# Performance work log

Measured on AMD Instinct MI355X. Metric: run time of the kernel, lower is better.

The kernel has to match this reference:

```python
import jax, jax.numpy as jnp
import numpy as np

N_NODES = 100000


def setup_inputs() -> dict:
    key = jax.random.key(0)
    k1, k2, k3 = jax.random.split(key, 3)
    embedding = jax.random.normal(k1, (N_NODES, 128), dtype=jnp.float32)
    # xavier-ish scale for 128-dim fan-in
    weights = jax.random.normal(k2, (2, 4, 128, 128), dtype=jnp.float32) * 0.088
    biases = jnp.zeros((2, 4, 128), dtype=jnp.float32)
    edges = jax.random.randint(k3, (4, 2, 150000), 0, N_NODES, dtype=jnp.int32)
    return {"embedding": embedding, "weights": weights, "biases": biases, "edges": edges}


def _hetero_conv(h, W, b, edges, n_nodes):
    """HeteroGraphConv(mean) over R relations; each GraphConv uses norm='both'.
    h: [N, d_in], W: [R, d_in, d_h], b: [R, d_h], edges: [R, 2, E]."""

    def per_rel(e, Wr, br):
        src, dst = e[0], e[1]
        ones = jnp.ones(src.shape, dtype=h.dtype)
        deg_out = jnp.maximum(jax.ops.segment_sum(ones, src, num_segments=n_nodes), 1.0)
        deg_in = jnp.maximum(jax.ops.segment_sum(ones, dst, num_segments=n_nodes), 1.0)
        # D_src^{-1/2} X W
        x = h * jax.lax.rsqrt(deg_out)[:, None]
        m = x @ Wr  # [N, d_h]
        # gather along edges, scatter-add to dst (A @ m)
        agg = jax.ops.segment_sum(m[src], dst, num_segments=n_nodes)
        return agg * jax.lax.rsqrt(deg_in)[:, None] + br

    outs = jax.vmap(per_rel)(edges, W, b)  # [R, N, d_h]
    return outs.mean(axis=0)


def reference(embedding, weights, biases, edges):
    n_nodes = embedding.shape[0]
    num_layers = weights.shape[0]
    h = embedding
    for i in range(num_layers):
        out = _hetero_conv(h, weights[i], biases[i], edges, n_nodes)
        out = jax.nn.leaky_relu(out, negative_slope=0.2)
        if i > 0:
            out = out + h  # residual (hidden == in, slice [:, :hidden] is identity)
        h = out
    return h
```

## Files before the change

### kernel.cpp

```cpp
#include <hip/hip_runtime.h>
#include <cstdint>
#include <cstddef>

#define N_NODES 100000
#define D 128
#define R 4
#define NE 150000
#define LAYERS 2
#define NROWS (R * N_NODES)
#define CAP 16
#define OVFS 12
#define TILES (N_NODES / 16)
#define GRID 256
#define TPB 512

typedef __attribute__((ext_vector_type(8))) short bf16x8;
typedef __attribute__((ext_vector_type(4))) float f32x4;
typedef __attribute__((ext_vector_type(4))) int i32x4;
typedef __attribute__((ext_vector_type(4))) unsigned short u16x4;

__device__ __forceinline__ unsigned short f2bf(float x) {
  union { float f; unsigned int u; } v; v.f = x;
  unsigned int u = v.u;
  return (unsigned short)((u + 0x7fffu + ((u >> 16) & 1u)) >> 16);
}
__device__ __forceinline__ float bf2f(unsigned short u) {
  union { unsigned int i; float f; } v; v.i = ((unsigned int)u) << 16;
  return v.f;
}

__global__ void prep1_kernel(const float* __restrict__ emb, const float* __restrict__ W,
                             const float* __restrict__ biases, const int* __restrict__ edges,
                             int* __restrict__ deg_i, unsigned short* __restrict__ hb,
                             unsigned short* __restrict__ Wt, float* __restrict__ bmean) {
  int t = blockIdx.x * blockDim.x + threadIdx.x;
  if (t < N_NODES * D / 4) {
    f32x4 v = *(const f32x4*)(emb + (size_t)t * 4);
    u16x4 o;
#pragma unroll
    for (int j = 0; j < 4; ++j) o[j] = f2bf(v[j]);
    *(u16x4*)(hb + (size_t)t * 4) = o;
  }
  if (t < NE * R) {
    int r = t / NE;
    int e = t - r * NE;
    int src = edges[(size_t)(r * 2) * NE + e];
    atomicAdd(&deg_i[r * N_NODES + src], 1);
  }
  if (t < LAYERS * R * D * D) {
    int k = t & 127;
    int c = (t >> 7) & 127;
    int lr = t >> 14;
    Wt[((size_t)lr << 14) | (c << 7) | k] = f2bf(W[((size_t)lr << 14) | (k << 7) | c]);
  }
  if (t < LAYERS * D) {
    int l = t >> 7, cc = t & 127;
    float s = 0.f;
    for (int r = 0; r < R; ++r) s += biases[((size_t)l * R + r) * D + cc];
    bmean[t] = s * 0.25f;
  }
}

__global__ void fill_kernel(const int* __restrict__ edges, const int* __restrict__ deg_i,
                            int* __restrict__ cursor, int2* __restrict__ rec2,
                            int2* __restrict__ ovf) {
  int e = blockIdx.x * blockDim.x + threadIdx.x;
  int r = blockIdx.y;
  if (e >= NE) return;
  int src = edges[(size_t)(r * 2) * NE + e];
  int dst = edges[(size_t)(r * 2 + 1) * NE + e];
  float sc = rsqrtf(fmaxf((float)deg_i[r * N_NODES + src], 1.0f));
  int rowg = r * N_NODES + dst;
  int slot = atomicAdd(&cursor[rowg], 1);
  if (slot < 4) {
    rec2[(((size_t)(r * TILES + (dst >> 4)) * 16 + (dst & 15)) << 2) + slot] =
        make_int2(src, __float_as_int(sc));
  } else if (slot < CAP) {
    ovf[(size_t)rowg * OVFS + (slot - 4)] = make_int2(src, __float_as_int(sc));
  }
}

__global__ __launch_bounds__(TPB, 2) void fused_kernel(
    const unsigned short* __restrict__ hb,
    const int2* __restrict__ rec2,
    const int2* __restrict__ ovf,
    const int* __restrict__ cnt,
    const unsigned short* __restrict__ Wt,
    const float* __restrict__ bmean,
    const unsigned short* __restrict__ resid_bf,
    float* __restrict__ out_f,
    unsigned short* __restrict__ out_bf) {
  __shared__ unsigned short t_lds[2][R * 4 * 64 * 8];
  const int w = threadIdx.x >> 6;
  const int lane = threadIdx.x & 63;
  const int m = lane & 15;
  const int q = lane >> 4;
  const int bid = blockIdx.x;
  const int nt = (TILES - bid + GRID - 1) / GRID;

  if (w < 4) {
    const int r = w;
    for (int it = 0; it < nt + 1; ++it) {
      if (it < nt) {
        const int tile = bid + it * GRID;
        const int rowg = r * N_NODES + tile * 16 + m;
        const int2* rp = rec2 + (((size_t)(r * TILES + tile) * 16 + m) << 2);
        int n = cnt[rowg];
        n = (n > CAP) ? CAP : n;
        i32x4 r01 = *(const i32x4*)(rp);
        i32x4 r23 = *(const i32x4*)(rp + 2);
        int   srcs[4] = { r01.x, r01.z, r23.x, r23.z };
        float scs[4]  = { __int_as_float(r01.y), __int_as_float(r01.w),
                          __int_as_float(r23.y), __int_as_float(r23.w) };
#pragma unroll
        for (int e = 0; e < 4; ++e) {
          if (e >= n) { srcs[e] = 0; scs[e] = 0.f; }
        }
        float accf[4][8];
#pragma unroll
        for (int ks = 0; ks < 4; ++ks)
#pragma unroll
          for (int j = 0; j < 8; ++j) accf[ks][j] = 0.f;
#pragma unroll
        for (int e = 0; e < 4; ++e) {
          const unsigned short* hp = hb + (size_t)srcs[e] * D + q * 8;
#pragma unroll
          for (int ks = 0; ks < 4; ++ks) {
            bf16x8 a = *(const bf16x8*)(hp + ks * 32);
#pragma unroll
            for (int j = 0; j < 8; ++j)
              accf[ks][j] += scs[e] * bf2f((unsigned short)a[j]);
          }
        }
        if (__builtin_expect(n > 4, 0)) {
          const int2* op = ovf + (size_t)rowg * OVFS;
          for (int i = 4; i < n; i += 2) {
            i32x4 rr = *(const i32x4*)(op + (i - 4));
            bool pairOk = (i + 1) < n;
            int  sA = rr.x;
            int  sB = pairOk ? rr.z : 0;
            float c0 = __int_as_float(rr.y);
            float c1 = pairOk ? __int_as_float(rr.w) : 0.f;
            const unsigned short* h0 = hb + (size_t)sA * D + q * 8;
            const unsigned short* h1 = hb + (size_t)sB * D + q * 8;
#pragma unroll
            for (int ks = 0; ks < 4; ++ks) {
              bf16x8 a0 = *(const bf16x8*)(h0 + ks * 32);
              bf16x8 a1 = *(const bf16x8*)(h1 + ks * 32);
#pragma unroll
              for (int j = 0; j < 8; ++j)
                accf[ks][j] += c0 * bf2f((unsigned short)a0[j]) + c1 * bf2f((unsigned short)a1[j]);
            }
          }
        }
        unsigned short* dstp = &t_lds[it & 1][(((r * 4) << 6) + lane) * 8];
#pragma unroll
        for (int ks = 0; ks < 4; ++ks) {
          union { bf16x8 v; unsigned short s[8]; } u;
#pragma unroll
          for (int j = 0; j < 8; ++j) u.s[j] = f2bf(accf[ks][j]);
          *(bf16x8*)(dstp + (ks << 6) * 8) = u.v;
        }
      }
      __syncthreads();
    }
  } else {
    const int cw = w - 4;
    bf16x8 breg[R][4][2];
#pragma unroll
    for (int r = 0; r < R; ++r) {
      const unsigned short* wr = Wt + ((size_t)r << 14);
#pragma unroll
      for (int ks = 0; ks < 4; ++ks)
#pragma unroll
        for (int c = 0; c < 2; ++c) {
          int ct = cw * 2 + c;
          breg[r][ks][c] = *(const bf16x8*)(wr + ((ct * 16 + m) << 7) + ks * 32 + q * 8);
        }
    }
    for (int it = 0; it < nt + 1; ++it) {
      if (it > 0) {
        const int tile = bid + (it - 1) * GRID;
        const int pb = (it - 1) & 1;
        float oacc[2][4];
#pragma unroll
        for (int c = 0; c < 2; ++c)
#pragma unroll
          for (int i = 0; i < 4; ++i) oacc[c][i] = 0.f;
#pragma unroll
        for (int r = 0; r < R; ++r) {
          f32x4 acc2[2];
#pragma unroll
          for (int c = 0; c < 2; ++c) acc2[c] = (f32x4){0.f, 0.f, 0.f, 0.f};
#pragma unroll
          for (int ks = 0; ks < 4; ++ks) {
            bf16x8 a = *(const bf16x8*)&t_lds[pb][(((r * 4 + ks) << 6) + lane) * 8];
#pragma unroll
            for (int c = 0; c < 2; ++c)
              acc2[c] = __builtin_amdgcn_mfma_f32_16x16x32_bf16(a, breg[r][ks][c], acc2[c], 0, 0, 0);
          }
          i32x4 ci = *(const i32x4*)(cnt + (size_t)r * N_NODES + tile * 16 + q * 4);
#pragma unroll
          for (int c = 0; c < 2; ++c)
#pragma unroll
            for (int i = 0; i < 4; ++i)
              oacc[c][i] += rsqrtf(fmaxf((float)ci[i], 1.0f)) * acc2[c][i];
        }
#pragma unroll
        for (int c = 0; c < 2; ++c) {
          int colx = (cw * 2 + c) * 16 + m;
          float bm = bmean[colx];
#pragma unroll
          for (int i = 0; i < 4; ++i) {
            int row = tile * 16 + q * 4 + i;
            float v = oacc[c][i] * 0.25f + bm;
            v = (v >= 0.f) ? v : 0.2f * v;
            if (resid_bf) v += bf2f(resid_bf[(size_t)row * D + colx]);
            if (out_f) out_f[(size_t)row * D + colx] = v;
            else       out_bf[(size_t)row * D + colx] = f2bf(v);
          }
        }
      }
      __syncthreads();
    }
  }
}

extern "C" void kernel_launch(void* const* d_in, const int* in_sizes, int n_in,
                              void* d_out, int out_size, void* d_ws, size_t ws_size,
                              hipStream_t stream) {
  const float* emb    = (const float*)d_in[0];
  const float* W      = (const float*)d_in[1];
  const float* biases = (const float*)d_in[2];
  const int*   edges  = (const int*)d_in[3];
  float* out = (float*)d_out;
  char* ws = (char*)d_ws;

  size_t off = 0;
  auto alloc = [&](size_t bytes) { size_t o = off; off += (bytes + 255) & ~255ull; return o; };
  int* ints      = (int*)(ws + alloc((size_t)2 * NROWS * 4));
  int* deg_i     = ints;
  int* cursor    = ints + NROWS;
  size_t zero_bytes = off;
  int2* rec2     = (int2*)(ws + alloc((size_t)R * TILES * 16 * 4 * 8));
  int2* ovf      = (int2*)(ws + alloc((size_t)NROWS * OVFS * 8));
  unsigned short* hb  = (unsigned short*)(ws + alloc((size_t)N_NODES * D * 2));
  unsigned short* hb2 = (unsigned short*)(ws + alloc((size_t)N_NODES * D * 2));
  unsigned short* Wt  = (unsigned short*)(ws + alloc((size_t)LAYERS * R * D * D * 2));
  float* bmean   = (float*)(ws + alloc((size_t)LAYERS * D * 4));
  (void)ws_size;

  hipMemsetAsync(ws, 0, zero_bytes, stream);
  prep1_kernel<<<(N_NODES * D / 4 + 255) / 256, 256, 0, stream>>>(
      emb, W, biases, edges, deg_i, hb, Wt, bmean);
  fill_kernel<<<dim3((NE + 255) / 256, R), 256, 0, stream>>>(edges, deg_i, cursor, rec2, ovf);

  fused_kernel<<<GRID, TPB, 0, stream>>>(
      hb, rec2, ovf, cursor, Wt, bmean, nullptr, nullptr, hb2);
  fused_kernel<<<GRID, TPB, 0, stream>>>(
      hb2, rec2, ovf, cursor, Wt + (size_t)R * D * D, bmean + D, hb2, out, nullptr);
}
```

Baseline: 340.1 us.

## Split fused warp-specialized kernel into separate aggregation and GEMM kernels

Replaces the warp-specialized fused kernel, where four gather waves fed four MFMA waves through double-buffered LDS, with two kernels. A fully parallel aggregation kernel writes bf16 aggregates for every relation to a global buffer, and a GEMM kernel then reads them back. The in-degree scaling moves into the aggregation step so the GEMM can accumulate across relations directly. This removes per-tile __syncthreads coupling and raises occupancy for the gather, at the cost of about 100MB of extra global traffic per layer plus two more launches.

```diff
diff --git a/kernel.cpp b/kernel.cpp
--- a/kernel.cpp
+++ b/kernel.cpp
@@ -11,8 +11,8 @@
 #define CAP 16
 #define OVFS 12
 #define TILES (N_NODES / 16)
-#define GRID 256
-#define TPB 512
+#define AGG_BLOCKS ((R * TILES) / 8)
+#define GEMM_BLOCKS 1024
 
 typedef __attribute__((ext_vector_type(8))) short bf16x8;
 typedef __attribute__((ext_vector_type(4))) float f32x4;
@@ -80,148 +80,138 @@
   }
 }
 
-__global__ __launch_bounds__(TPB, 2) void fused_kernel(
-    const unsigned short* __restrict__ hb,
+__global__ __launch_bounds__(512, 4) void agg_kernel(
+    const unsigned short* __restrict__ hin,
     const int2* __restrict__ rec2,
     const int2* __restrict__ ovf,
     const int* __restrict__ cnt,
+    unsigned short* __restrict__ agg) {
+  const int gw = (blockIdx.x * blockDim.x + threadIdx.x) >> 6;
+  const int lane = threadIdx.x & 63;
+  const int m = lane & 15;
+  const int q = lane >> 4;
+  const int rel = gw / TILES;
+  const int tile = gw - rel * TILES;
+
+  const int rowg = rel * N_NODES + tile * 16 + m;
+  const int2* rp = rec2 + (((size_t)gw * 16 + m) << 2);
+  int cn = cnt[rowg];
+  int n = cn > CAP ? CAP : cn;
+  float sin_ = rsqrtf(fmaxf((float)cn, 1.0f));
+  i32x4 r01 = *(const i32x4*)(rp);
+  i32x4 r23 = *(const i32x4*)(rp + 2);
+  int   srcs[4] = { r01.x, r01.z, r23.x, r23.z };
+  float scs[4]  = { __int_as_float(r01.y), __int_as_float(r01.w),
+                    __int_as_float(r23.y), __int_as_float(r23.w) };
+#pragma unroll
+  for (int e = 0; e < 4; ++e) {
+    if (e >= n) { srcs[e] = 0; scs[e] = 0.f; }
+  }
+  float accf[4][8];
+#pragma unroll
+  for (int ks = 0; ks < 4; ++ks)
+#pragma unroll
+    for (int j = 0; j < 8; ++j) accf[ks][j] = 0.f;
+#pragma unroll
+  for (int e = 0; e < 4; ++e) {
+    const unsigned short* hp = hin + (size_t)srcs[e] * D + q * 8;
+#pragma unroll
+    for (int ks = 0; ks < 4; ++ks) {
+      bf16x8 a = *(const bf16x8*)(hp + ks * 32);
+#pragma unroll
+      for (int j = 0; j < 8; ++j)
+        accf[ks][j] += scs[e] * bf2f((unsigned short)a[j]);
+    }
+  }
+  if (__builtin_expect(n > 4, 0)) {
+    const int2* op = ovf + (size_t)rowg * OVFS;
+    for (int i = 4; i < n; i += 2) {
+      i32x4 rr = *(const i32x4*)(op + (i - 4));
+      bool pairOk = (i + 1) < n;
+      int  sA = rr.x;
+      int  sB = pairOk ? rr.z : 0;
+      float c0 = __int_as_float(rr.y);
+      float c1 = pairOk ? __int_as_float(rr.w) : 0.f;
+      const unsigned short* h0 = hin + (size_t)sA * D + q * 8;
+      const unsigned short* h1 = hin + (size_t)sB * D + q * 8;
+#pragma unroll
+      for (int ks = 0; ks < 4; ++ks) {
+        bf16x8 a0 = *(const bf16x8*)(h0 + ks * 32);
+        bf16x8 a1 = *(const bf16x8*)(h1 + ks * 32);
+#pragma unroll
+        for (int j = 0; j < 8; ++j)
+          accf[ks][j] += c0 * bf2f((unsigned short)a0[j]) + c1 * bf2f((unsigned short)a1[j]);
+      }
+    }
+  }
+  unsigned short* dstp = agg + (((size_t)gw * 4) * 64 + lane) * 8;
+#pragma unroll
+  for (int ks = 0; ks < 4; ++ks) {
+    union { bf16x8 v; unsigned short s[8]; } u;
+#pragma unroll
+    for (int j = 0; j < 8; ++j) u.s[j] = f2bf(accf[ks][j] * sin_);
+    *(bf16x8*)(dstp + (size_t)ks * 64 * 8) = u.v;
+  }
+}
+
+__global__ __launch_bounds__(256, 2) void gemm_kernel(
+    const unsigned short* __restrict__ agg,
     const unsigned short* __restrict__ Wt,
     const float* __restrict__ bmean,
     const unsigned short* __restrict__ resid_bf,
     float* __restrict__ out_f,
     unsigned short* __restrict__ out_bf) {
-  __shared__ unsigned short t_lds[2][R * 4 * 64 * 8];
   const int w = threadIdx.x >> 6;
   const int lane = threadIdx.x & 63;
   const int m = lane & 15;
   const int q = lane >> 4;
-  const int bid = blockIdx.x;
-  const int nt = (TILES - bid + GRID - 1) / GRID;
-
-  if (w < 4) {
-    const int r = w;
-    for (int it = 0; it < nt + 1; ++it) {
-      if (it < nt) {
-        const int tile = bid + it * GRID;
-        const int rowg = r * N_NODES + tile * 16 + m;
-        const int2* rp = rec2 + (((size_t)(r * TILES + tile) * 16 + m) << 2);
-        int n = cnt[rowg];
-        n = (n > CAP) ? CAP : n;
-        i32x4 r01 = *(const i32x4*)(rp);
-        i32x4 r23 = *(const i32x4*)(rp + 2);
-        int   srcs[4] = { r01.x, r01.z, r23.x, r23.z };
-        float scs[4]  = { __int_as_float(r01.y), __int_as_float(r01.w),
-                          __int_as_float(r23.y), __int_as_float(r23.w) };
-#pragma unroll
-        for (int e = 0; e < 4; ++e) {
-          if (e >= n) { srcs[e] = 0; scs[e] = 0.f; }
-        }
-        float accf[4][8];
-#pragma unroll
-        for (int ks = 0; ks < 4; ++ks)
-#pragma unroll
-          for (int j = 0; j < 8; ++j) accf[ks][j] = 0.f;
-#pragma unroll
-        for (int e = 0; e < 4; ++e) {
-          const unsigned short* hp = hb + (size_t)srcs[e] * D + q * 8;
-#pragma unroll
-          for (int ks = 0; ks < 4; ++ks) {
-            bf16x8 a = *(const bf16x8*)(hp + ks * 32);
-#pragma unroll
-            for (int j = 0; j < 8; ++j)
-              accf[ks][j] += scs[e] * bf2f((unsigned short)a[j]);
-          }
-        }
-        if (__builtin_expect(n > 4, 0)) {
-          const int2* op = ovf + (size_t)rowg * OVFS;
-          for (int i = 4; i < n; i += 2) {
-            i32x4 rr = *(const i32x4*)(op + (i - 4));
-            bool pairOk = (i + 1) < n;
-            int  sA = rr.x;
-            int  sB = pairOk ? rr.z : 0;
-            float c0 = __int_as_float(rr.y);
-            float c1 = pairOk ? __int_as_float(rr.w) : 0.f;
-            const unsigned short* h0 = hb + (size_t)sA * D + q * 8;
-            const unsigned short* h1 = hb + (size_t)sB * D + q * 8;
-#pragma unroll
-            for (int ks = 0; ks < 4; ++ks) {
-              bf16x8 a0 = *(const bf16x8*)(h0 + ks * 32);
-              bf16x8 a1 = *(const bf16x8*)(h1 + ks * 32);
-#pragma unroll
-              for (int j = 0; j < 8; ++j)
-                accf[ks][j] += c0 * bf2f((unsigned short)a0[j]) + c1 * bf2f((unsigned short)a1[j]);
-            }
-          }
-        }
-        unsigned short* dstp = &t_lds[it & 1][(((r * 4) << 6) + lane) * 8];
-#pragma unroll
-        for (int ks = 0; ks < 4; ++ks) {
-          union { bf16x8 v; unsigned short s[8]; } u;
-#pragma unroll
-          for (int j = 0; j < 8; ++j) u.s[j] = f2bf(accf[ks][j]);
-          *(bf16x8*)(dstp + (ks << 6) * 8) = u.v;
-        }
-      }
-      __syncthreads();
-    }
-  } else {
-    const int cw = w - 4;
-    bf16x8 breg[R][4][2];
+
+  bf16x8 breg[R][4][2];
+#pragma unroll
+  for (int r = 0; r < R; ++r) {
+    const unsigned short* wr = Wt + ((size_t)r << 14);
+#pragma unroll
+    for (int ks = 0; ks < 4; ++ks)
+#pragma unroll
+      for (int c = 0; c < 2; ++c) {
+        int ct = w * 2 + c;
+        breg[r][ks][c] = *(const bf16x8*)(wr + ((ct * 16 + m) << 7) + ks * 32 + q * 8);
+      }
+  }
+
+  for (int tile = blockIdx.x; tile < TILES; tile += GEMM_BLOCKS) {
+    f32x4 acc[2];
+#pragma unroll
+    for (int c = 0; c < 2; ++c) acc[c] = (f32x4){0.f, 0.f, 0.f, 0.f};
 #pragma unroll
     for (int r = 0; r < R; ++r) {
-      const unsigned short* wr = Wt + ((size_t)r << 14);
-#pragma unroll
-      for (int ks = 0; ks < 4; ++ks)
-#pragma unroll
-        for (int c = 0; c < 2; ++c) {
-          int ct = cw * 2 + c;
-          breg[r][ks][c] = *(const bf16x8*)(wr + ((ct * 16 + m) << 7) + ks * 32 + q * 8);
-        }
-    }
-    for (int it = 0; it < nt + 1; ++it) {
-      if (it > 0) {
-        const int tile = bid + (it - 1) * GRID;
-        const int pb = (it - 1) & 1;
-        float oacc[2][4];
-#pragma unroll
-        for (int c = 0; c < 2; ++c)
-#pragma unroll
-          for (int i = 0; i < 4; ++i) oacc[c][i] = 0.f;
-#pragma unroll
-        for (int r = 0; r < R; ++r) {
-          f32x4 acc2[2];
-#pragma unroll
-          for (int c = 0; c < 2; ++c) acc2[c] = (f32x4){0.f, 0.f, 0.f, 0.f};
-#pragma unroll
-          for (int ks = 0; ks < 4; ++ks) {
-            bf16x8 a = *(const bf16x8*)&t_lds[pb][(((r * 4 + ks) << 6) + lane) * 8];
-#pragma unroll
-            for (int c = 0; c < 2; ++c)
-              acc2[c] = __builtin_amdgcn_mfma_f32_16x16x32_bf16(a, breg[r][ks][c], acc2[c], 0, 0, 0);
-          }
-          i32x4 ci = *(const i32x4*)(cnt + (size_t)r * N_NODES + tile * 16 + q * 4);
-#pragma unroll
-          for (int c = 0; c < 2; ++c)
-#pragma unroll
-            for (int i = 0; i < 4; ++i)
-              oacc[c][i] += rsqrtf(fmaxf((float)ci[i], 1.0f)) * acc2[c][i];
-        }
-#pragma unroll
-        for (int c = 0; c < 2; ++c) {
-          int colx = (cw * 2 + c) * 16 + m;
-          float bm = bmean[colx];
-#pragma unroll
-          for (int i = 0; i < 4; ++i) {
-            int row = tile * 16 + q * 4 + i;
-            float v = oacc[c][i] * 0.25f + bm;
-            v = (v >= 0.f) ? v : 0.2f * v;
-            if (resid_bf) v += bf2f(resid_bf[(size_t)row * D + colx]);
-            if (out_f) out_f[(size_t)row * D + colx] = v;
-            else       out_bf[(size_t)row * D + colx] = f2bf(v);
-          }
-        }
-      }
-      __syncthreads();
+      const unsigned short* ap =
+          agg + ((size_t)(r * TILES + tile) * 256 + lane) * 8;
+      bf16x8 a0 = *(const bf16x8*)(ap);
+      bf16x8 a1 = *(const bf16x8*)(ap + 512);
+      bf16x8 a2 = *(const bf16x8*)(ap + 1024);
+      bf16x8 a3 = *(const bf16x8*)(ap + 1536);
+#pragma unroll
+      for (int c = 0; c < 2; ++c) {
+        acc[c] = __builtin_amdgcn_mfma_f32_16x16x32_bf16(a0, breg[r][0][c], acc[c], 0, 0, 0);
+        acc[c] = __builtin_amdgcn_mfma_f32_16x16x32_bf16(a1, breg[r][1][c], acc[c], 0, 0, 0);
+        acc[c] = __builtin_amdgcn_mfma_f32_16x16x32_bf16(a2, breg[r][2][c], acc[c], 0, 0, 0);
+        acc[c] = __builtin_amdgcn_mfma_f32_16x16x32_bf16(a3, breg[r][3][c], acc[c], 0, 0, 0);
+      }
+    }
+#pragma unroll
+    for (int c = 0; c < 2; ++c) {
+      int colx = (w * 2 + c) * 16 + m;
+      float bm = bmean[colx];
+#pragma unroll
+      for (int i = 0; i < 4; ++i) {
+        int row = tile * 16 + q * 4 + i;
+        float v = acc[c][i] * 0.25f + bm;
+        v = (v >= 0.f) ? v : 0.2f * v;
+        if (resid_bf) v += bf2f(resid_bf[(size_t)row * D + colx]);
+        if (out_f) out_f[(size_t)row * D + colx] = v;
+        else       out_bf[(size_t)row * D + colx] = f2bf(v);
+      }
     }
   }
 }
@@ -248,6 +238,7 @@
   unsigned short* hb2 = (unsigned short*)(ws + alloc((size_t)N_NODES * D * 2));
   unsigned short* Wt  = (unsigned short*)(ws + alloc((size_t)LAYERS * R * D * D * 2));
   float* bmean   = (float*)(ws + alloc((size_t)LAYERS * D * 4));
+  unsigned short* agg = (unsigned short*)(ws + alloc((size_t)R * N_NODES * D * 2));
   (void)ws_size;
 
   hipMemsetAsync(ws, 0, zero_bytes, stream);
@@ -255,8 +246,9 @@
       emb, W, biases, edges, deg_i, hb, Wt, bmean);
   fill_kernel<<<dim3((NE + 255) / 256, R), 256, 0, stream>>>(edges, deg_i, cursor, rec2, ovf);
 
-  fused_kernel<<<GRID, TPB, 0, stream>>>(
-      hb, rec2, ovf, cursor, Wt, bmean, nullptr, nullptr, hb2);
-  fused_kernel<<<GRID, TPB, 0, stream>>>(
-      hb2, rec2, ovf, cursor, Wt + (size_t)R * D * D, bmean + D, hb2, out, nullptr);
-}
+  agg_kernel<<<AGG_BLOCKS, 512, 0, stream>>>(hb, rec2, ovf, cursor, agg);
+  gemm_kernel<<<GEMM_BLOCKS, 256, 0, stream>>>(agg, Wt, bmean, nullptr, nullptr, hb2);
+  agg_kernel<<<AGG_BLOCKS, 512, 0, stream>>>(hb2, rec2, ovf, cursor, agg);
+  gemm_kernel<<<GEMM_BLOCKS, 256, 0, stream>>>(agg, Wt + (size_t)R * D * D, bmean + D,
+                                               hb2, out, nullptr);
+}
```

Result: slower. 376.8 us (+10.8%).
